# Optimization experiments

Measured on AMD Instinct MI355X. Metric: run time of the kernel, lower is better.

The kernel has to match this reference:

```python
import jax, jax.numpy as jnp
from jax import lax
import numpy as np

NUM_INST = 32   # upper bound on instance ids (segment count)
B, H, W = 2, 512, 1024
FM = 16         # featuremap_count (hard-coded in module)
DS = 4          # downsample_count
DN = ('NCHW', 'OIHW', 'NCHW')
EPS = 1e-5


def conv(x, w, b, stride, pad, reflect=False):
    if reflect:
        x = jnp.pad(x, ((0, 0), (0, 0), (pad, pad), (pad, pad)), mode='reflect')
        padding = 'VALID'
    else:
        padding = ((pad, pad), (pad, pad))
    y = lax.conv_general_dilated(x, w, (stride, stride), padding, dimension_numbers=DN)
    return y + b[None, :, None, None]


def conv_transpose(x, w, b):
    # PyTorch ConvTranspose2d(k=3, s=2, p=1, output_padding=1) == dilated conv with
    # flipped kernel, lhs_dilation=2, asymmetric padding (1, 2) -> output 2*H
    wr = w[:, :, ::-1, ::-1]
    y = lax.conv_general_dilated(x, wr, (1, 1), ((1, 2), (1, 2)),
                                 lhs_dilation=(2, 2), dimension_numbers=DN)
    return y + b[None, :, None, None]


def instance_norm(x):
    mu = jnp.mean(x, axis=(2, 3), keepdims=True)
    var = jnp.var(x, axis=(2, 3), keepdims=True)
    return (x - mu) * lax.rsqrt(var + EPS)


def average_pool(x, inst):
    # Per-image, per-instance mean over pixels, broadcast back (segment mean).
    Bq, C, Hq, Wq = x.shape
    ids = inst[:, 0].reshape(Bq, Hq * Wq)       # [B, HW] int segment ids
    flat = x.reshape(Bq, C, Hq * Wq)

    def per_image(xf, idf):                      # xf: [C, HW], idf: [HW]
        sums = jax.ops.segment_sum(xf.T, idf, num_segments=NUM_INST)   # [NUM_INST, C]
        cnts = jax.ops.segment_sum(jnp.ones_like(idf, xf.dtype), idf,
                                   num_segments=NUM_INST)              # [NUM_INST]
        means = sums / jnp.maximum(cnts, 1.0)[:, None]
        return means[idf].T                      # gather mean back to pixels [C, HW]

    return jax.vmap(per_image)(flat, ids).reshape(Bq, C, Hq, Wq)


def setup_inputs() -> dict:
    key = jax.random.key(0)
    ks = iter(jax.random.split(key, 64))
    inp = {}
    inp['input_tensor'] = jax.random.normal(next(ks), (B, 3, H, W), jnp.float32)
    inp['instance_map'] = jax.random.randint(next(ks), (B, 1, H, W), 0, NUM_INST)

    def wb(cout, cin, k):
        w = jax.random.normal(next(ks), (cout, cin, k, k), jnp.float32) / np.sqrt(cin * k * k)
        b = jax.random.normal(next(ks), (cout,), jnp.float32) * 0.01
        return w, b

    chans = [FM * 2 ** i for i in range(DS + 1)]  # 16, 32, 64, 128, 256
    inp['e0_w'], inp['e0_b'] = wb(FM, 3, 7)
    for i in range(DS):
        inp[f'e{i + 1}_w'], inp[f'e{i + 1}_b'] = wb(chans[i + 1], chans[i], 3)
    for i in range(DS):
        inp[f'd{i}_w'], inp[f'd{i}_b'] = wb(chans[DS - i - 1], chans[DS - i], 3)
    inp['d4_w'], inp['d4_b'] = wb(3, FM, 7)
    return inp


def reference(input_tensor, instance_map,
              e0_w, e0_b, e1_w, e1_b, e2_w, e2_b, e3_w, e3_b, e4_w, e4_b,
              d0_w, d0_b, d1_w, d1_b, d2_w, d2_b, d3_w, d3_b, d4_w, d4_b):
    # Encoder: reflect-pad 7x7 conv then 4 stride-2 downsampling convs (IN + ReLU)
    x = jax.nn.relu(instance_norm(conv(input_tensor, e0_w, e0_b, 1, 3, reflect=True)))
    for w, b in ((e1_w, e1_b), (e2_w, e2_b), (e3_w, e3_b), (e4_w, e4_b)):
        x = jax.nn.relu(instance_norm(conv(x, w, b, 2, 1)))
    # Decoder: 4 stride-2 transpose convs (IN + ReLU), final reflect-pad 7x7 conv (no norm/relu)
    for w, b in ((d0_w, d0_b), (d1_w, d1_b), (d2_w, d2_b), (d3_w, d3_b)):
        x = jax.nn.relu(instance_norm(conv_transpose(x, w, b)))
    x = conv(x, d4_w, d4_b, 1, 3, reflect=True)
    x = jnp.tanh(x)
    return average_pool(x, instance_map)
```

## Files before the change

### kernel.cpp

```cpp
#include <hip/hip_runtime.h>
#include <cstddef>

#define NUM_INST 32
#define EPS_IN 1e-5f

__device__ __forceinline__ int reflect_idx(int i, int n) {
    if (i < 0) i = -i;
    else if (i >= n) i = 2 * n - 2 - i;
    return i;
}

template<int CIN, int COUT, int NCH, bool NORM, bool TANH>
__global__ void __launch_bounds__(256, 4)
conv7_lds(const float* __restrict__ x, const float* __restrict__ w,
          const float* __restrict__ bias,
          const float* __restrict__ mu, const float* __restrict__ rs,
          float* __restrict__ y, int H, int W)
{
    constexpr int COUTP = (COUT + 3) & ~3;
    __shared__ float wsm[CIN * 49 * COUTP];
    __shared__ float tile[NCH][38 * 39];
    __shared__ float smu[CIN], srs[CIN];
    const int tid = threadIdx.x;
    const int b = blockIdx.z;

    for (int idx = tid; idx < CIN * 49 * COUTP; idx += 256) {
        int ocp = idx % COUTP;
        int r   = idx / COUTP;
        wsm[idx] = (ocp < COUT) ? w[(size_t)ocp * CIN * 49 + r] : 0.f;
    }
    if (NORM && tid < CIN) { smu[tid] = mu[b * CIN + tid]; srs[tid] = rs[b * CIN + tid]; }

    const int oh_base = blockIdx.y * 32, ow_base = blockIdx.x * 32;
    const int ohl = tid >> 3, owl0 = (tid & 7) * 4;

    float acc[4][COUT];
#pragma unroll
    for (int o = 0; o < COUT; ++o) {
        float bv = bias[o];
#pragma unroll
        for (int j = 0; j < 4; ++j) acc[j][o] = bv;
    }

    for (int ic0 = 0; ic0 < CIN; ic0 += NCH) {
        __syncthreads();
        for (int idx = tid; idx < NCH * 1444; idx += 256) {
            int c = idx / 1444;
            int rr = idx % 1444;
            int r = rr / 38, col = rr % 38;
            int gy = reflect_idx(oh_base - 3 + r, H);
            int gx = reflect_idx(ow_base - 3 + col, W);
            float v = x[((size_t)(b * CIN + ic0 + c)) * H * W + (size_t)gy * W + gx];
            if (NORM) v = fmaxf((v - smu[ic0 + c]) * srs[ic0 + c], 0.f);
            tile[c][r * 39 + col] = v;
        }
        __syncthreads();
#pragma unroll
        for (int cc = 0; cc < NCH; ++cc) {
            const float* tp = &tile[cc][0];
            const float4* wp4 = (const float4*)&wsm[(ic0 + cc) * 49 * COUTP];
#pragma unroll
            for (int kh = 0; kh < 7; ++kh) {
                float rv[10];
#pragma unroll
                for (int i = 0; i < 10; ++i) rv[i] = tp[(ohl + kh) * 39 + owl0 + i];
#pragma unroll
                for (int kw = 0; kw < 7; ++kw) {
#pragma unroll
                    for (int o4 = 0; o4 < COUTP / 4; ++o4) {
                        float4 wv = wp4[(kh * 7 + kw) * (COUTP / 4) + o4];
#pragma unroll
                        for (int j = 0; j < 4; ++j) {
                            if (o4 * 4 + 0 < COUT) acc[j][o4 * 4 + 0] += rv[kw + j] * wv.x;
                            if (o4 * 4 + 1 < COUT) acc[j][o4 * 4 + 1] += rv[kw + j] * wv.y;
                            if (o4 * 4 + 2 < COUT) acc[j][o4 * 4 + 2] += rv[kw + j] * wv.z;
                            if (o4 * 4 + 3 < COUT) acc[j][o4 * 4 + 3] += rv[kw + j] * wv.w;
                        }
                    }
                }
            }
        }
    }

    const int oh = oh_base + ohl, ow0 = ow_base + owl0;
#pragma unroll
    for (int o = 0; o < COUT; ++o) {
        float4 st;
        st.x = acc[0][o]; st.y = acc[1][o]; st.z = acc[2][o]; st.w = acc[3][o];
        if (TANH) { st.x = tanhf(st.x); st.y = tanhf(st.y); st.z = tanhf(st.z); st.w = tanhf(st.w); }
        *(float4*)&y[(((size_t)b * COUT + o) * H + oh) * W + ow0] = st;
    }
}

template<int CIN, int COUT, int OCPT, int KS, bool NORM>
__global__ void __launch_bounds__(256)
conv3_s2(const float* __restrict__ x, const float* __restrict__ w,
         const float* __restrict__ bias,
         const float* __restrict__ mu, const float* __restrict__ rs,
         float* __restrict__ y, size_t ystride, int Hin, int Win)
{
    const int Hout = Hin >> 1, Wout = Win >> 1;
    constexpr int CK = CIN / KS;
    __shared__ float wsm[CK * 9 * OCPT];
    __shared__ float smu[CIN], srs[CIN];
    const int tid = threadIdx.x;
    const int NG = COUT / OCPT;
    const int z = blockIdx.z;
    const int ks = z % KS;
    const int ogb = z / KS;
    const int b = ogb / NG, g = ogb % NG;
    const int oc0 = g * OCPT;
    const int icbase = ks * CK;
    for (int idx = tid; idx < CK * 9 * OCPT; idx += 256) {
        int o = idx % OCPT;
        int r = idx / OCPT;
        wsm[idx] = w[(size_t)(oc0 + o) * CIN * 9 + (size_t)icbase * 9 + r];
    }
    if (NORM && tid < CIN) { smu[tid] = mu[b * CIN + tid]; srs[tid] = rs[b * CIN + tid]; }
    __syncthreads();

    const int ow = blockIdx.x * 16 + (tid & 15);
    const int oh = blockIdx.y * 16 + (tid >> 4);

    float acc[OCPT];
#pragma unroll
    for (int o = 0; o < OCPT; ++o) acc[o] = (ks == 0) ? bias[oc0 + o] : 0.f;

    for (int icl = 0; icl < CK; ++icl) {
        const int ic = icbase + icl;
        const float* xp = x + ((size_t)(b * CIN + ic)) * Hin * Win;
        float m = NORM ? smu[ic] : 0.f;
        float rr = NORM ? srs[ic] : 0.f;
#pragma unroll
        for (int kh = 0; kh < 3; ++kh) {
            int ih = 2 * oh + kh - 1;
            if (ih < 0 || ih >= Hin) continue;
#pragma unroll
            for (int kw = 0; kw < 3; ++kw) {
                int iw = 2 * ow + kw - 1;
                if (iw < 0 || iw >= Win) continue;
                float v = xp[(size_t)ih * Win + iw];
                if (NORM) v = fmaxf((v - m) * rr, 0.f);
                const float* wp = &wsm[(icl * 9 + kh * 3 + kw) * OCPT];
#pragma unroll
                for (int o = 0; o < OCPT; ++o) acc[o] += wp[o] * v;
            }
        }
    }
    float* yb = y + (size_t)ks * ystride;
    float* yp = yb + (((size_t)b * COUT + oc0) * Hout + oh) * Wout + ow;
#pragma unroll
    for (int o = 0; o < OCPT; ++o) yp[(size_t)o * Hout * Wout] = acc[o];
}

template<int CIN, int COUT, int ICB, int KS>
__global__ void __launch_bounds__(256)
tconv3_v2(const float* __restrict__ x, const float* __restrict__ w,
          const float* __restrict__ bias,
          const float* __restrict__ mu, const float* __restrict__ rs,
          float* __restrict__ y, size_t ystride, int Hin, int Win)
{
    constexpr int OCB = 16;
    constexpr int NOG = COUT / OCB;
    constexpr int CK = CIN / KS;
    const int z = blockIdx.z;
    const int ks = z % KS;
    const int ogb = z / KS;
    const int b = ogb / NOG;
    const int ocb = (ogb % NOG) * OCB;
    const int r0 = blockIdx.y * 8, c0 = blockIdx.x * 32;
    const int Hout = Hin * 2, Wout = Win * 2;

    __shared__ float xt[ICB][9 * 36];
    __shared__ float wt[ICB][9][OCB];
    __shared__ float smu[CIN], srs[CIN];

    const int tid = threadIdx.x;
    if (tid < CIN) { smu[tid] = mu[b * CIN + tid]; srs[tid] = rs[b * CIN + tid]; }

    const int tid_s = tid & 63;
    const int og = tid >> 6;
    const int sr = tid_s >> 3;
    const int sc4 = (tid_s & 7) * 4;

    float acc[4][4][4];
#pragma unroll
    for (int o = 0; o < 4; ++o) {
        float bv = (ks == 0) ? bias[ocb + og * 4 + o] : 0.f;
#pragma unroll
        for (int pr = 0; pr < 4; ++pr)
#pragma unroll
            for (int p = 0; p < 4; ++p) acc[pr][o][p] = bv;
    }

    for (int ic0 = ks * CK; ic0 < (ks + 1) * CK; ic0 += ICB) {
        __syncthreads();
        for (int idx = tid; idx < ICB * 9 * 33; idx += 256) {
            int c  = idx / (9 * 33);
            int rr = idx % (9 * 33);
            int r  = rr / 33, col = rr % 33;
            int gr = r0 + r, gc = c0 + col;
            int ic = ic0 + c;
            float v = 0.f;
            if (gr < Hin && gc < Win) {
                v = x[((size_t)(b * CIN + ic)) * Hin * Win + (size_t)gr * Win + gc];
                v = fmaxf((v - smu[ic]) * srs[ic], 0.f);
            }
            xt[c][r * 36 + col] = v;
        }
        for (int idx = tid; idx < ICB * 9 * OCB; idx += 256) {
            int oc  = idx & (OCB - 1);
            int tap = (idx >> 4) % 9;
            int c   = idx / (9 * OCB);
            wt[c][tap][oc] = w[(size_t)(ocb + oc) * CIN * 9 + (size_t)(ic0 + c) * 9 + tap];
        }
        __syncthreads();

#pragma unroll 4
        for (int c = 0; c < ICB; ++c) {
            const float* xr = &xt[c][sr * 36 + sc4];
            float x0[5], x1[5];
            {
                float4 a = *(const float4*)xr;
                x0[0] = a.x; x0[1] = a.y; x0[2] = a.z; x0[3] = a.w; x0[4] = xr[4];
                float4 bq = *(const float4*)(xr + 36);
                x1[0] = bq.x; x1[1] = bq.y; x1[2] = bq.z; x1[3] = bq.w; x1[4] = xr[40];
            }
            const float* wp = &wt[c][0][og * 4];
#define TAPFMA(TAP, PAR, XV, SH)                                                   \
            {                                                                      \
                float4 wq = *(const float4*)(wp + (TAP) * OCB);                    \
                float wv[4] = {wq.x, wq.y, wq.z, wq.w};                            \
                _Pragma("unroll")                                                  \
                for (int o = 0; o < 4; ++o)                                        \
                    _Pragma("unroll")                                              \
                    for (int p = 0; p < 4; ++p)                                    \
                        acc[PAR][o][p] += wv[o] * XV[p + SH];                      \
            }
            TAPFMA(4, 0, x0, 0)
            TAPFMA(5, 1, x0, 0)
            TAPFMA(3, 1, x0, 1)
            TAPFMA(7, 2, x0, 0)
            TAPFMA(1, 2, x1, 0)
            TAPFMA(8, 3, x0, 0)
            TAPFMA(6, 3, x0, 1)
            TAPFMA(2, 3, x1, 0)
            TAPFMA(0, 3, x1, 1)
#undef TAPFMA
        }
    }

    float* yb = y + (size_t)ks * ystride;
    const int gr = r0 + sr, gc = c0 + sc4;
#pragma unroll
    for (int o = 0; o < 4; ++o) {
        int oc = ocb + og * 4 + o;
        float* yp = yb + (((size_t)(b * COUT + oc)) * Hout + 2 * gr) * Wout + 2 * gc;
        float4 e0, e1, d0, d1;
        e0.x = acc[0][o][0]; e0.y = acc[1][o][0]; e0.z = acc[0][o][1]; e0.w = acc[1][o][1];
        e1.x = acc[0][o][2]; e1.y = acc[1][o][2]; e1.z = acc[0][o][3]; e1.w = acc[1][o][3];
        d0.x = acc[2][o][0]; d0.y = acc[3][o][0]; d0.z = acc[2][o][1]; d0.w = acc[3][o][1];
        d1.x = acc[2][o][2]; d1.y = acc[3][o][2]; d1.z = acc[2][o][3]; d1.w = acc[3][o][3];
        *(float4*)yp = e0;
        *(float4*)(yp + 4) = e1;
        *(float4*)(yp + Wout) = d0;
        *(float4*)(yp + Wout + 4) = d1;
    }
}

template<int KS>
__global__ void __launch_bounds__(256)
reduce_stats(const float* __restrict__ parts, size_t pstride,
             float* __restrict__ out, float* __restrict__ acc, int HW)
{
    const int bc = blockIdx.x;
    const int chunk = HW / gridDim.y;
    const size_t base = (size_t)bc * HW + (size_t)blockIdx.y * chunk;
    float s = 0.f, ss = 0.f;
    const int n4 = chunk >> 2;
    for (int i = threadIdx.x; i < n4; i += 256) {
        float4 v = ((const float4*)(parts + base))[i];
#pragma unroll
        for (int k = 1; k < KS; ++k) {
            float4 u = ((const float4*)(parts + (size_t)k * pstride + base))[i];
            v.x += u.x; v.y += u.y; v.z += u.z; v.w += u.w;
        }
        ((float4*)(out + base))[i] = v;
        s += v.x + v.y + v.z + v.w;
        ss += v.x * v.x + v.y * v.y + v.z * v.z + v.w * v.w;
    }
#pragma unroll
    for (int off = 32; off; off >>= 1) {
        s += __shfl_down(s, off);
        ss += __shfl_down(ss, off);
    }
    __shared__ float rbuf[8];
    const int wid = threadIdx.x >> 6;
    if ((threadIdx.x & 63) == 0) { rbuf[wid] = s; rbuf[4 + wid] = ss; }
    __syncthreads();
    if (threadIdx.x == 0) {
        s = rbuf[0] + rbuf[1] + rbuf[2] + rbuf[3];
        ss = rbuf[4] + rbuf[5] + rbuf[6] + rbuf[7];
        atomicAdd(&acc[bc], s);
        atomicAdd(&acc[512 + bc], ss);
    }
}

__global__ void __launch_bounds__(256)
in_stats_partial(const float* __restrict__ y, float* __restrict__ acc, int HW)
{
    const int bc = blockIdx.x;
    const int chunk = HW / gridDim.y;
    const float* p = y + (size_t)bc * HW + (size_t)blockIdx.y * chunk;
    float s = 0.f, ss = 0.f;
    const float4* p4 = (const float4*)p;
    const int n4 = chunk >> 2;
    for (int i = threadIdx.x; i < n4; i += 256) {
        float4 v = p4[i];
        s += v.x + v.y + v.z + v.w;
        ss += v.x * v.x + v.y * v.y + v.z * v.z + v.w * v.w;
    }
#pragma unroll
    for (int off = 32; off; off >>= 1) {
        s += __shfl_down(s, off);
        ss += __shfl_down(ss, off);
    }
    __shared__ float rbuf[8];
    const int wid = threadIdx.x >> 6;
    if ((threadIdx.x & 63) == 0) { rbuf[wid] = s; rbuf[4 + wid] = ss; }
    __syncthreads();
    if (threadIdx.x == 0) {
        s = rbuf[0] + rbuf[1] + rbuf[2] + rbuf[3];
        ss = rbuf[4] + rbuf[5] + rbuf[6] + rbuf[7];
        atomicAdd(&acc[bc], s);
        atomicAdd(&acc[512 + bc], ss);
    }
}

__global__ void in_stats_final(const float* __restrict__ acc,
                               float* __restrict__ mu, float* __restrict__ rs,
                               int BC, float invHW)
{
    int i = blockIdx.x * 256 + threadIdx.x;
    if (i < BC) {
        float m = acc[i] * invHW;
        float var = fmaxf(acc[512 + i] * invHW - m * m, 0.f);
        mu[i] = m;
        rs[i] = rsqrtf(var + EPS_IN);
    }
}

__global__ void zero_ws_k(float* __restrict__ p, int n)
{
    int i = blockIdx.x * 256 + threadIdx.x;
    if (i < n) p[i] = 0.f;
}

__global__ void __launch_bounds__(256)
seg_accum(const float* __restrict__ yT, const int* __restrict__ inst,
          float* __restrict__ seg, int HW)
{
    const int b = blockIdx.y;
    __shared__ float ls[NUM_INST * 4];
    if (threadIdx.x < NUM_INST * 4) ls[threadIdx.x] = 0.f;
    __syncthreads();
    const float* p0 = yT + (size_t)b * 3 * HW;
    const int* ip = inst + (size_t)b * HW;
    for (int i = blockIdx.x * 256 + threadIdx.x; i < HW; i += gridDim.x * 256) {
        int id = ip[i];
        atomicAdd(&ls[id * 4 + 0], p0[i]);
        atomicAdd(&ls[id * 4 + 1], p0[HW + i]);
        atomicAdd(&ls[id * 4 + 2], p0[2 * (size_t)HW + i]);
        atomicAdd(&ls[id * 4 + 3], 1.f);
    }
    __syncthreads();
    if (threadIdx.x < NUM_INST * 4)
        atomicAdd(&seg[b * NUM_INST * 4 + threadIdx.x], ls[threadIdx.x]);
}

__global__ void seg_means_k(const float* __restrict__ seg, float* __restrict__ means)
{
    int i = threadIdx.x;
    if (i < 2 * NUM_INST * 3) {
        int bi = i / 3, c = i % 3;
        float cnt = seg[bi * 4 + 3];
        means[i] = seg[bi * 4 + c] / fmaxf(cnt, 1.f);
    }
}

__global__ void __launch_bounds__(256)
seg_scatter(const int* __restrict__ inst, const float* __restrict__ means,
            float* __restrict__ out, int HW)
{
    const int b = blockIdx.y;
    for (int i = blockIdx.x * 256 + threadIdx.x; i < HW; i += gridDim.x * 256) {
        int id = inst[(size_t)b * HW + i];
        const float* m = &means[(b * NUM_INST + id) * 3];
        out[((size_t)b * 3 + 0) * HW + i] = m[0];
        out[((size_t)b * 3 + 1) * HW + i] = m[1];
        out[((size_t)b * 3 + 2) * HW + i] = m[2];
    }
}

extern "C" void kernel_launch(void* const* d_in, const int* in_sizes, int n_in,
                              void* d_out, int out_size, void* d_ws, size_t ws_size,
                              hipStream_t stream)
{
    const float* x_in = (const float*)d_in[0];
    const int* inst = (const int*)d_in[1];
    const float* e0w = (const float*)d_in[2];  const float* e0b = (const float*)d_in[3];
    const float* e1w = (const float*)d_in[4];  const float* e1b = (const float*)d_in[5];
    const float* e2w = (const float*)d_in[6];  const float* e2b = (const float*)d_in[7];
    const float* e3w = (const float*)d_in[8];  const float* e3b = (const float*)d_in[9];
    const float* e4w = (const float*)d_in[10]; const float* e4b = (const float*)d_in[11];
    const float* d0w = (const float*)d_in[12]; const float* d0b = (const float*)d_in[13];
    const float* d1w = (const float*)d_in[14]; const float* d1b = (const float*)d_in[15];
    const float* d2w = (const float*)d_in[16]; const float* d2b = (const float*)d_in[17];
    const float* d3w = (const float*)d_in[18]; const float* d3b = (const float*)d_in[19];
    const float* d4w = (const float*)d_in[20]; const float* d4b = (const float*)d_in[21];
    float* outp = (float*)d_out;

    float* bufA = (float*)d_ws;
    float* bufB = bufA + 16777216;
    float* st   = bufB + 8388608;
    float* acc  = st + 9 * 1024;
    float* seg  = acc + 9 * 1024;
    float* means = seg + 2 * NUM_INST * 4;

    const dim3 blk(256);
    const int H = 512, W = 1024;

    {
        int nz = 9 * 1024 + 2 * NUM_INST * 4;
        zero_ws_k<<<dim3((nz + 255) / 256), blk, 0, stream>>>(acc, nz);
    }

#define STATS(buf, L, C, HWv)                                                        \
    in_stats_partial<<<dim3(2 * (C), 8), blk, 0, stream>>>((buf), acc + (L) * 1024, (HWv)); \
    in_stats_final<<<dim3(2), blk, 0, stream>>>(acc + (L) * 1024, st + (L) * 1024,          \
                                                st + (L) * 1024 + 512, 2 * (C),             \
                                                1.0f / (HWv));

    conv7_lds<3, 16, 3, false, false><<<dim3(W / 32, H / 32, 2), blk, 0, stream>>>(
        x_in, e0w, e0b, nullptr, nullptr, bufA, H, W);
    STATS(bufA, 0, 16, H * W);

    conv3_s2<16, 32, 8, 1, true><<<dim3(32, 16, 2 * 4), blk, 0, stream>>>(
        bufA, e1w, e1b, st + 0 * 1024, st + 0 * 1024 + 512, bufB, 0, 512, 1024);
    STATS(bufB, 1, 32, 256 * 512);

    conv3_s2<32, 64, 8, 1, true><<<dim3(16, 8, 2 * 8), blk, 0, stream>>>(
        bufB, e2w, e2b, st + 1 * 1024, st + 1 * 1024 + 512, bufA, 0, 256, 512);
    STATS(bufA, 2, 64, 128 * 256);

    {
        const size_t PS = 2097152;
        float* parts = bufB + 2097152;
        conv3_s2<64, 128, 8, 2, true><<<dim3(8, 4, 2 * 16 * 2), blk, 0, stream>>>(
            bufA, e3w, e3b, st + 2 * 1024, st + 2 * 1024 + 512, parts, PS, 128, 256);
        reduce_stats<2><<<dim3(2 * 128, 8), blk, 0, stream>>>(
            parts, PS, bufB, acc + 3 * 1024, 64 * 128);
        in_stats_final<<<dim3(2), blk, 0, stream>>>(acc + 3 * 1024, st + 3 * 1024,
                                                    st + 3 * 1024 + 512, 2 * 128,
                                                    1.0f / (64 * 128));
    }

    {
        const size_t PS = 1048576;
        float* parts = bufA + 1048576;
        conv3_s2<128, 256, 8, 4, true><<<dim3(4, 2, 2 * 32 * 4), blk, 0, stream>>>(
            bufB, e4w, e4b, st + 3 * 1024, st + 3 * 1024 + 512, parts, PS, 64, 128);
        reduce_stats<4><<<dim3(2 * 256, 8), blk, 0, stream>>>(
            parts, PS, bufA, acc + 4 * 1024, 32 * 64);
        in_stats_final<<<dim3(2), blk, 0, stream>>>(acc + 4 * 1024, st + 4 * 1024,
                                                    st + 4 * 1024 + 512, 2 * 256,
                                                    1.0f / (32 * 64));
    }

    {
        const size_t PS = 2097152;
        float* parts = bufA + 2097152;
        tconv3_v2<256, 128, 16, 4><<<dim3(2, 4, 2 * 8 * 4), blk, 0, stream>>>(
            bufA, d0w, d0b, st + 4 * 1024, st + 4 * 1024 + 512, parts, PS, 32, 64);
        reduce_stats<4><<<dim3(2 * 128, 8), blk, 0, stream>>>(
            parts, PS, bufB, acc + 5 * 1024, 64 * 128);
        in_stats_final<<<dim3(2), blk, 0, stream>>>(acc + 5 * 1024, st + 5 * 1024,
                                                    st + 5 * 1024 + 512, 2 * 128,
                                                    1.0f / (64 * 128));
    }

    {
        const size_t PS = 4194304;
        float* parts = bufA + 8388608;
        tconv3_v2<128, 64, 16, 2><<<dim3(4, 8, 2 * 4 * 2), blk, 0, stream>>>(
            bufB, d1w, d1b, st + 5 * 1024, st + 5 * 1024 + 512, parts, PS, 64, 128);
        reduce_stats<2><<<dim3(2 * 64, 8), blk, 0, stream>>>(
            parts, PS, bufA, acc + 6 * 1024, 128 * 256);
        in_stats_final<<<dim3(2), blk, 0, stream>>>(acc + 6 * 1024, st + 6 * 1024,
                                                    st + 6 * 1024 + 512, 2 * 64,
                                                    1.0f / (128 * 256));
    }

    tconv3_v2<64, 32, 16, 1><<<dim3(8, 16, 2 * 2), blk, 0, stream>>>(
        bufA, d2w, d2b, st + 6 * 1024, st + 6 * 1024 + 512, bufB, 0, 128, 256);
    STATS(bufB, 7, 32, 256 * 512);

    tconv3_v2<32, 16, 16, 1><<<dim3(16, 32, 2), blk, 0, stream>>>(
        bufB, d3w, d3b, st + 7 * 1024, st + 7 * 1024 + 512, bufA, 0, 256, 512);
    STATS(bufA, 8, 16, H * W);

    conv7_lds<16, 3, 4, true, true><<<dim3(W / 32, H / 32, 2), blk, 0, stream>>>(
        bufA, d4w, d4b, st + 8 * 1024, st + 8 * 1024 + 512, bufB, H, W);

    seg_accum<<<dim3(256, 2), blk, 0, stream>>>(bufB, inst, seg, H * W);
    seg_means_k<<<dim3(1), blk, 0, stream>>>(seg, means);
    seg_scatter<<<dim3(512, 2), blk, 0, stream>>>(inst, means, outp, H * W);

#undef STATS
}
```

Baseline: 1.075 ms.

## Fuse IN stats into late tconvs and fuse final conv with segment accumulation

```diff
diff --git a/kernel.cpp b/kernel.cpp
--- a/kernel.cpp
+++ b/kernel.cpp
@@ -8,6 +8,12 @@
     if (i < 0) i = -i;
     else if (i >= n) i = 2 * n - 2 - i;
     return i;
+}
+
+__device__ __forceinline__ float tanh_fast(float v) {
+    float a = fminf(fmaxf(v, -9.f), 9.f);
+    float e = __expf(2.f * a);
+    return (e - 1.f) / (e + 1.f);
 }
 
 template<int CIN, int COUT, int NCH, bool NORM, bool TANH>
@@ -90,6 +96,95 @@
         if (TANH) { st.x = tanhf(st.x); st.y = tanhf(st.y); st.z = tanhf(st.z); st.w = tanhf(st.w); }
         *(float4*)&y[(((size_t)b * COUT + o) * H + oh) * W + ow0] = st;
     }
+}
+
+template<int CIN, int NCH>
+__global__ void __launch_bounds__(256, 4)
+conv7_seg(const float* __restrict__ x, const float* __restrict__ w,
+          const float* __restrict__ bias,
+          const float* __restrict__ mu, const float* __restrict__ rs,
+          const int* __restrict__ inst, float* __restrict__ seg, int H, int W)
+{
+    __shared__ float wsm[CIN * 49 * 4];
+    __shared__ float tile[NCH][38 * 71];
+    __shared__ float smu[CIN], srs[CIN];
+    __shared__ float ls[NUM_INST * 4];
+    const int tid = threadIdx.x;
+    const int b = blockIdx.z;
+
+    if (tid < NUM_INST * 4) ls[tid] = 0.f;
+    for (int idx = tid; idx < CIN * 49 * 4; idx += 256) {
+        int ocp = idx & 3;
+        int r   = idx >> 2;
+        wsm[idx] = (ocp < 3) ? w[(size_t)ocp * CIN * 49 + r] : 0.f;
+    }
+    if (tid < CIN) { smu[tid] = mu[b * CIN + tid]; srs[tid] = rs[b * CIN + tid]; }
+
+    const int oh_base = blockIdx.y * 32, ow_base = blockIdx.x * 64;
+    const int row = tid >> 3;
+    const int col8 = (tid & 7) * 8;
+
+    float acc[8][3];
+#pragma unroll
+    for (int c = 0; c < 3; ++c) {
+        float bv = bias[c];
+#pragma unroll
+        for (int j = 0; j < 8; ++j) acc[j][c] = bv;
+    }
+
+    for (int ic0 = 0; ic0 < CIN; ic0 += NCH) {
+        __syncthreads();
+        for (int idx = tid; idx < NCH * 38 * 70; idx += 256) {
+            int c  = idx / (38 * 70);
+            int rr = idx % (38 * 70);
+            int r  = rr / 70, cl = rr % 70;
+            int gy = reflect_idx(oh_base - 3 + r, H);
+            int gx = reflect_idx(ow_base - 3 + cl, W);
+            int ic = ic0 + c;
+            float v = x[((size_t)(b * CIN + ic)) * H * W + (size_t)gy * W + gx];
+            v = fmaxf((v - smu[ic]) * srs[ic], 0.f);
+            tile[c][r * 71 + cl] = v;
+        }
+        __syncthreads();
+#pragma unroll
+        for (int cc = 0; cc < NCH; ++cc) {
+            const float* tp = &tile[cc][0];
+            const float4* wp4 = (const float4*)&wsm[(ic0 + cc) * 49 * 4];
+#pragma unroll
+            for (int kh = 0; kh < 7; ++kh) {
+                float rv[14];
+#pragma unroll
+                for (int i = 0; i < 14; ++i) rv[i] = tp[(row + kh) * 71 + col8 + i];
+#pragma unroll
+                for (int kw = 0; kw < 7; ++kw) {
+                    float4 wv = wp4[kh * 7 + kw];
+#pragma unroll
+                    for (int j = 0; j < 8; ++j) {
+                        acc[j][0] += rv[kw + j] * wv.x;
+                        acc[j][1] += rv[kw + j] * wv.y;
+                        acc[j][2] += rv[kw + j] * wv.z;
+                    }
+                }
+            }
+        }
+    }
+
+    const int oh = oh_base + row, ow0 = ow_base + col8;
+    const int* ip = inst + (size_t)b * H * W + (size_t)oh * W + ow0;
+    int4 ia = *(const int4*)ip;
+    int4 ib = *(const int4*)(ip + 4);
+    int idv[8] = {ia.x, ia.y, ia.z, ia.w, ib.x, ib.y, ib.z, ib.w};
+#pragma unroll
+    for (int j = 0; j < 8; ++j) {
+        int base = idv[j] * 4;
+        atomicAdd(&ls[base + 0], tanh_fast(acc[j][0]));
+        atomicAdd(&ls[base + 1], tanh_fast(acc[j][1]));
+        atomicAdd(&ls[base + 2], tanh_fast(acc[j][2]));
+        atomicAdd(&ls[base + 3], 1.f);
+    }
+    __syncthreads();
+    if (tid < NUM_INST * 4)
+        atomicAdd(&seg[b * NUM_INST * 4 + tid], ls[tid]);
 }
 
 template<int CIN, int COUT, int OCPT, int KS, bool NORM>
@@ -153,12 +248,13 @@
     for (int o = 0; o < OCPT; ++o) yp[(size_t)o * Hout * Wout] = acc[o];
 }
 
-template<int CIN, int COUT, int ICB, int KS>
+template<int CIN, int COUT, int ICB, int KS, bool DOSTATS>
 __global__ void __launch_bounds__(256)
 tconv3_v2(const float* __restrict__ x, const float* __restrict__ w,
           const float* __restrict__ bias,
           const float* __restrict__ mu, const float* __restrict__ rs,
-          float* __restrict__ y, size_t ystride, int Hin, int Win)
+          float* __restrict__ y, size_t ystride, int Hin, int Win,
+          float* __restrict__ sacc)
 {
     constexpr int OCB = 16;
     constexpr int NOG = COUT / OCB;
@@ -266,6 +362,38 @@
         *(float4*)(yp + Wout) = d0;
         *(float4*)(yp + Wout + 4) = d1;
     }
+
+    if (DOSTATS) {
+        float s[4], q[4];
+#pragma unroll
+        for (int o = 0; o < 4; ++o) {
+            s[o] = 0.f; q[o] = 0.f;
+#pragma unroll
+            for (int pr = 0; pr < 4; ++pr)
+#pragma unroll
+                for (int p = 0; p < 4; ++p) {
+                    float v = acc[pr][o][p];
+                    s[o] += v;
+                    q[o] += v * v;
+                }
+        }
+#pragma unroll
+        for (int off = 32; off; off >>= 1) {
+#pragma unroll
+            for (int o = 0; o < 4; ++o) {
+                s[o] += __shfl_down(s[o], off);
+                q[o] += __shfl_down(q[o], off);
+            }
+        }
+        if (tid_s == 0) {
+#pragma unroll
+            for (int o = 0; o < 4; ++o) {
+                int bc = b * COUT + ocb + og * 4 + o;
+                atomicAdd(&sacc[bc], s[o]);
+                atomicAdd(&sacc[512 + bc], q[o]);
+            }
+        }
+    }
 }
 
 template<int KS>
@@ -354,28 +482,6 @@
 {
     int i = blockIdx.x * 256 + threadIdx.x;
     if (i < n) p[i] = 0.f;
-}
-
-__global__ void __launch_bounds__(256)
-seg_accum(const float* __restrict__ yT, const int* __restrict__ inst,
-          float* __restrict__ seg, int HW)
-{
-    const int b = blockIdx.y;
-    __shared__ float ls[NUM_INST * 4];
-    if (threadIdx.x < NUM_INST * 4) ls[threadIdx.x] = 0.f;
-    __syncthreads();
-    const float* p0 = yT + (size_t)b * 3 * HW;
-    const int* ip = inst + (size_t)b * HW;
-    for (int i = blockIdx.x * 256 + threadIdx.x; i < HW; i += gridDim.x * 256) {
-        int id = ip[i];
-        atomicAdd(&ls[id * 4 + 0], p0[i]);
-        atomicAdd(&ls[id * 4 + 1], p0[HW + i]);
-        atomicAdd(&ls[id * 4 + 2], p0[2 * (size_t)HW + i]);
-        atomicAdd(&ls[id * 4 + 3], 1.f);
-    }
-    __syncthreads();
-    if (threadIdx.x < NUM_INST * 4)
-        atomicAdd(&seg[b * NUM_INST * 4 + threadIdx.x], ls[threadIdx.x]);
 }
 
 __global__ void seg_means_k(const float* __restrict__ seg, float* __restrict__ means)
@@ -480,8 +586,9 @@
     {
         const size_t PS = 2097152;
         float* parts = bufA + 2097152;
-        tconv3_v2<256, 128, 16, 4><<<dim3(2, 4, 2 * 8 * 4), blk, 0, stream>>>(
-            bufA, d0w, d0b, st + 4 * 1024, st + 4 * 1024 + 512, parts, PS, 32, 64);
+        tconv3_v2<256, 128, 16, 4, false><<<dim3(2, 4, 2 * 8 * 4), blk, 0, stream>>>(
+            bufA, d0w, d0b, st + 4 * 1024, st + 4 * 1024 + 512, parts, PS, 32, 64,
+            nullptr);
         reduce_stats<4><<<dim3(2 * 128, 8), blk, 0, stream>>>(
             parts, PS, bufB, acc + 5 * 1024, 64 * 128);
         in_stats_final<<<dim3(2), blk, 0, stream>>>(acc + 5 * 1024, st + 5 * 1024,
@@ -492,8 +599,9 @@
     {
         const size_t PS = 4194304;
         float* parts = bufA + 8388608;
-        tconv3_v2<128, 64, 16, 2><<<dim3(4, 8, 2 * 4 * 2), blk, 0, stream>>>(
-            bufB, d1w, d1b, st + 5 * 1024, st + 5 * 1024 + 512, parts, PS, 64, 128);
+        tconv3_v2<128, 64, 16, 2, false><<<dim3(4, 8, 2 * 4 * 2), blk, 0, stream>>>(
+            bufB, d1w, d1b, st + 5 * 1024, st + 5 * 1024 + 512, parts, PS, 64, 128,
+            nullptr);
         reduce_stats<2><<<dim3(2 * 64, 8), blk, 0, stream>>>(
             parts, PS, bufA, acc + 6 * 1024, 128 * 256);
         in_stats_final<<<dim3(2), blk, 0, stream>>>(acc + 6 * 1024, st + 6 * 1024,
@@ -501,18 +609,23 @@
                                                     1.0f / (128 * 256));
     }
 
-    tconv3_v2<64, 32, 16, 1><<<dim3(8, 16, 2 * 2), blk, 0, stream>>>(
-        bufA, d2w, d2b, st + 6 * 1024, st + 6 * 1024 + 512, bufB, 0, 128, 256);
-    STATS(bufB, 7, 32, 256 * 512);
-
-    tconv3_v2<32, 16, 16, 1><<<dim3(16, 32, 2), blk, 0, stream>>>(
-        bufB, d3w, d3b, st + 7 * 1024, st + 7 * 1024 + 512, bufA, 0, 256, 512);
-    STATS(bufA, 8, 16, H * W);
-
-    conv7_lds<16, 3, 4, true, true><<<dim3(W / 32, H / 32, 2), blk, 0, stream>>>(
-        bufA, d4w, d4b, st + 8 * 1024, st + 8 * 1024 + 512, bufB, H, W);
-
-    seg_accum<<<dim3(256, 2), blk, 0, stream>>>(bufB, inst, seg, H * W);
+    tconv3_v2<64, 32, 16, 1, true><<<dim3(8, 16, 2 * 2), blk, 0, stream>>>(
+        bufA, d2w, d2b, st + 6 * 1024, st + 6 * 1024 + 512, bufB, 0, 128, 256,
+        acc + 7 * 1024);
+    in_stats_final<<<dim3(2), blk, 0, stream>>>(acc + 7 * 1024, st + 7 * 1024,
+                                                st + 7 * 1024 + 512, 2 * 32,
+                                                1.0f / (256 * 512));
+
+    tconv3_v2<32, 16, 16, 1, true><<<dim3(16, 32, 2), blk, 0, stream>>>(
+        bufB, d3w, d3b, st + 7 * 1024, st + 7 * 1024 + 512, bufA, 0, 256, 512,
+        acc + 8 * 1024);
+    in_stats_final<<<dim3(2), blk, 0, stream>>>(acc + 8 * 1024, st + 8 * 1024,
+                                                st + 8 * 1024 + 512, 2 * 16,
+                                                1.0f / (512 * 1024));
+
+    conv7_seg<16, 2><<<dim3(W / 64, H / 32, 2), blk, 0, stream>>>(
+        bufA, d4w, d4b, st + 8 * 1024, st + 8 * 1024 + 512, inst, seg, H, W);
+
     seg_means_k<<<dim3(1), blk, 0, stream>>>(seg, means);
     seg_scatter<<<dim3(512, 2), blk, 0, stream>>>(inst, means, outp, H * W);
 
```

Result: slower. 1.209 ms (+12.4%).
